# Kernel tuning notes

Measured on AMD Instinct MI355X. Metric: run time of the kernel, lower is better.

## Reference

```python
import jax, jax.numpy as jnp
import numpy as np

N_NODES = 50000
N_EDGES = 1600000
N_GRAPHS = 512
IN_DIM = 128
HID = 128          # nb_hidden
HALF = HID // 2    # per-branch GAT out dim
NEG_SLOPE = 0.2


def _glorot(key, shape):
    fan_in, fan_out = shape[0], shape[-1]
    lim = (6.0 / (fan_in + fan_out)) ** 0.5
    return jax.random.uniform(key, shape, jnp.float32, -lim, lim)


def setup_inputs() -> dict:
    key = jax.random.key(0)
    ks = jax.random.split(key, 32)
    inp = {
        "x": jax.random.normal(ks[0], (N_NODES, IN_DIM), jnp.float32),
        "edge_index": jax.random.randint(ks[1], (2, N_EDGES), 0, N_NODES, jnp.int64),
        "dense_edge_idx": jax.random.randint(ks[2], (2, N_EDGES), 0, N_NODES, jnp.int64),
        "batch": jnp.sort(jax.random.randint(ks[3], (N_NODES,), 0, N_GRAPHS, jnp.int64)),
    }
    # Shared GAT layers (layersB aliases layersA in the source!), nb_layer = 3
    in_dims = [IN_DIM, HID, HID]
    for i, d_in in enumerate(in_dims):
        inp[f"W{i}"] = _glorot(ks[4 + 4 * i], (d_in, HALF))
        inp[f"a_src{i}"] = _glorot(ks[5 + 4 * i], (1, HALF))[0]
        inp[f"a_dst{i}"] = _glorot(ks[6 + 4 * i], (1, HALF))[0]
        inp[f"b{i}"] = jnp.zeros((HALF,), jnp.float32)
    inp["Wf"] = _glorot(ks[20], (HID, 1))
    inp["bf"] = jnp.zeros((1,), jnp.float32)
    return inp


def _gat_conv(x, src, dst, W, a_src, a_dst, b):
    """PyG GATConv, heads=1, concat=True, add_self_loops=True."""
    n = x.shape[0]
    h = x @ W                                   # [N, HALF]
    loops = jnp.arange(n, dtype=src.dtype)
    s = jnp.concatenate([src, loops])           # [E+N]
    d = jnp.concatenate([dst, loops])
    e = (h @ a_src)[s] + (h @ a_dst)[d]         # per-edge raw score
    e = jnp.where(e >= 0, e, NEG_SLOPE * e)     # LeakyReLU(0.2)
    # segment softmax over destination nodes
    m = jax.ops.segment_max(e, d, num_segments=n)
    e = jnp.exp(e - m[d])
    z = jax.ops.segment_sum(e, d, num_segments=n)
    alpha = e / (z[d] + 1e-16)                  # [E+N]
    out = jax.ops.segment_sum(h[s] * alpha[:, None], d, num_segments=n)
    return out + b


def reference(x, edge_index, dense_edge_idx, batch,
              W0, a_src0, a_dst0, b0,
              W1, a_src1, a_dst1, b1,
              W2, a_src2, a_dst2, b2,
              Wf, bf):
    layers = [(W0, a_src0, a_dst0, b0), (W1, a_src1, a_dst1, b1), (W2, a_src2, a_dst2, b2)]
    for (W, a_s, a_d, b) in layers:
        x_A = _gat_conv(x, edge_index[0], edge_index[1], W, a_s, a_d, b)
        x_B = _gat_conv(x, dense_edge_idx[0], dense_edge_idx[1], W, a_s, a_d, b)
        x = jax.nn.relu(jnp.concatenate([x_A, x_B], axis=1))   # [N, HID]
    pooled = jax.ops.segment_sum(x, batch, num_segments=N_GRAPHS)  # [G, HID]
    y = (pooled @ Wf + bf).squeeze(-1)                             # [G]
    return y
```

## Files before the change

### kernel.cpp

```cpp
#include <hip/hip_runtime.h>
#include <hip/hip_bf16.h>
#include <hip/hip_fp16.h>

#define NEG_INF -3.4e38f
#define BCAP 9216

typedef _Float16 f16x8 __attribute__((ext_vector_type(8)));
typedef float f32x4 __attribute__((ext_vector_type(4)));

static __device__ __forceinline__ float leaky(float t) { return t >= 0.f ? t : 0.2f * t; }
static __device__ __forceinline__ __half2 i2h2(int v) { __half2 h; *(int*)&h = v; return h; }

__global__ __launch_bounds__(256) void bucket_k(const int* __restrict__ eiA, const int* __restrict__ eiB,
                                                int E, int nbkt, int* __restrict__ bktCnt,
                                                int* __restrict__ pairs,
                                                const float* __restrict__ W0, const float* __restrict__ W1,
                                                const float* __restrict__ W2, _Float16* __restrict__ Wt) {
    int t = threadIdx.x;
    if (blockIdx.x < 96) {
        int i = blockIdx.x * 256 + t;
        int l = i >> 13;
        int idx = i & 8191;
        int c = idx >> 7;
        int k = idx & 127;
        const float* W = (l == 0) ? W0 : (l == 1) ? W1 : W2;
        Wt[i] = (_Float16)W[k * 64 + c];
    }

    int KB = gridDim.x >> 1;
    int b = blockIdx.x;
    int sel = (b >= KB);
    int bb = sel ? b - KB : b;
    const int* src = sel ? eiB : eiA;
    const int* dst = src + E;
    int* bc = bktCnt + (sel ? nbkt : 0);
    int* pr = pairs + (size_t)(sel ? nbkt : 0) * BCAP;

    __shared__ int hist[256];
    hist[t] = 0;
    __syncthreads();

    int e0 = (int)(((long long)bb * E) / KB);
    int e1 = (int)(((long long)(bb + 1) * E) / KB);
    for (int i = e0 + t; i < e1; i += 256) atomicAdd(&hist[dst[i] >> 8], 1);
    __syncthreads();

    int h = hist[t];
    int base = h ? atomicAdd(&bc[t], h) : 0;
    __syncthreads();
    hist[t] = base;
    __syncthreads();

    for (int i = e0 + t; i < e1; i += 256) {
        int d = dst[i];
        int s = src[i];
        int bk = d >> 8;
        int pos = atomicAdd(&hist[bk], 1);
        if (pos < BCAP) pr[(size_t)bk * BCAP + pos] = s | ((d & 255) << 16);
    }
}

__global__ __launch_bounds__(256) void bscan_k(const int* __restrict__ bktCnt, const int* __restrict__ pairs,
                                               int N, int nbkt, int2* __restrict__ rpl2,
                                               int* __restrict__ bsum) {
    __shared__ int h[256];
    int b = blockIdx.x;
    int sel = (b >= nbkt);
    int bk = sel ? b - nbkt : b;
    const int* bc = bktCnt + (sel ? nbkt : 0);
    const int* pr = pairs + ((size_t)(sel ? nbkt : 0) + bk) * BCAP;
    int t = threadIdx.x;
    h[t] = 0;
    __syncthreads();
    int cb = min(bc[bk], BCAP);
    for (int i = t; i < cb; i += 256) atomicAdd(&h[pr[i] >> 16], 1);
    __syncthreads();
    int v = h[t];
#pragma unroll
    for (int off = 1; off < 256; off <<= 1) {
        int add = (t >= off) ? h[t - off] : 0;
        __syncthreads();
        h[t] += add;
        __syncthreads();
    }
    int node = (bk << 8) + t;
    if (node < N) rpl2[(sel ? N : 0) + node] = make_int2(h[t] - v, v);
    if (t == 255) bsum[b] = h[255];
}

__global__ __launch_bounds__(512) void scan2_k(int* __restrict__ bsum, int nb,
                                               float* __restrict__ y, const float* __restrict__ bf, int G) {
    __shared__ int s[512];
    int t = threadIdx.x;
    for (int g = t; g < G; g += 512) y[g] = bf[0];
    int seg = t >> 8;
    int j = t & 255;
    int v = (j < nb) ? bsum[seg * nb + j] : 0;
    s[t] = v;
    __syncthreads();
#pragma unroll
    for (int off = 1; off < 256; off <<= 1) {
        int add = (j >= off) ? s[t - off] : 0;
        __syncthreads();
        s[t] += add;
        __syncthreads();
    }
    if (j < nb) bsum[seg * nb + j] = s[t] - v;
}

__global__ __launch_bounds__(256) void bfill2_k(const int* __restrict__ bktCnt, const int* __restrict__ pairs,
                                                int N, int nbkt, const int2* __restrict__ rpl2,
                                                const int* __restrict__ bsum, int2* __restrict__ rp2,
                                                int* __restrict__ colA, int* __restrict__ colB) {
    __shared__ int curs[256];
    int b = blockIdx.x;
    int sel = (b >= nbkt);
    int bk = sel ? b - nbkt : b;
    const int* bc = bktCnt + (sel ? nbkt : 0);
    const int* pr = pairs + ((size_t)(sel ? nbkt : 0) + bk) * BCAP;
    int* col = sel ? colB : colA;
    int t = threadIdx.x;
    int base = bsum[b];
    int node = (bk << 8) + t;
    if (node < N) {
        int2 lv = rpl2[(sel ? N : 0) + node];
        int r0 = lv.x + base;
        rp2[(sel ? N : 0) + node] = make_int2(r0, lv.y);
        curs[t] = r0;
    }
    __syncthreads();
    int cb = min(bc[bk], BCAP);
    for (int i = t; i < cb; i += 256) {
        int pk = pr[i];
        int p = atomicAdd(&curs[pk >> 16], 1);
        col[p] = pk & 0xFFFF;
    }
}

template <int IN16>
__global__ __launch_bounds__(256) void gemm_k(const void* __restrict__ Xv, const _Float16* __restrict__ Wt,
                                              const float* __restrict__ asrc, const float* __restrict__ adst,
                                              _Float16* __restrict__ H16, float* __restrict__ es,
                                              float* __restrict__ ed, int N) {
    int tid = threadIdx.x;
    int w = tid >> 6;
    int lane = tid & 63;
    int l15 = lane & 15;
    int hi = lane >> 4;
    int rbase = blockIdx.x * 128 + w * 32;

    f32x4 acc[2][4] = {};
#pragma unroll
    for (int kc = 0; kc < 4; ++kc) {
        f16x8 a[2];
#pragma unroll
        for (int mt = 0; mt < 2; ++mt) {
            int r = min(rbase + mt * 16 + l15, N - 1);
            if (IN16) {
                const _Float16* X = (const _Float16*)Xv;
                a[mt] = *(const f16x8*)(X + (size_t)r * 128 + kc * 32 + hi * 8);
            } else {
                const float* px = (const float*)Xv + (size_t)r * 128 + kc * 32 + hi * 8;
                float4 x0 = *(const float4*)px;
                float4 x1 = *(const float4*)(px + 4);
                f16x8 t;
                t[0] = (_Float16)x0.x; t[1] = (_Float16)x0.y; t[2] = (_Float16)x0.z; t[3] = (_Float16)x0.w;
                t[4] = (_Float16)x1.x; t[5] = (_Float16)x1.y; t[6] = (_Float16)x1.z; t[7] = (_Float16)x1.w;
                a[mt] = t;
            }
        }
#pragma unroll
        for (int nt = 0; nt < 4; ++nt) {
            f16x8 bfrag = *(const f16x8*)(Wt + (size_t)(nt * 16 + l15) * 128 + kc * 32 + hi * 8);
            acc[0][nt] = __builtin_amdgcn_mfma_f32_16x16x32_f16(a[0], bfrag, acc[0][nt], 0, 0, 0);
            acc[1][nt] = __builtin_amdgcn_mfma_f32_16x16x32_f16(a[1], bfrag, acc[1][nt], 0, 0, 0);
        }
    }

    float av[4], dv[4];
#pragma unroll
    for (int nt = 0; nt < 4; ++nt) {
        av[nt] = asrc[nt * 16 + l15];
        dv[nt] = adst[nt * 16 + l15];
    }
#pragma unroll
    for (int mt = 0; mt < 2; ++mt) {
#pragma unroll
        for (int r = 0; r < 4; ++r) {
            int row = rbase + mt * 16 + hi * 4 + r;
            float s1 = 0.f, s2 = 0.f;
#pragma unroll
            for (int nt = 0; nt < 4; ++nt) {
                float v = acc[mt][nt][r];
                s1 += v * av[nt];
                s2 += v * dv[nt];
            }
#pragma unroll
            for (int off = 1; off < 16; off <<= 1) {
                s1 += __shfl_xor(s1, off, 64);
                s2 += __shfl_xor(s2, off, 64);
            }
            if (row < N) {
                if (l15 == 0) { es[row] = s1; ed[row] = s2; }
#pragma unroll
                for (int nt = 0; nt < 4; ++nt)
                    H16[(size_t)row * 64 + nt * 16 + l15] = (_Float16)acc[mt][nt][r];
            }
        }
    }
}

template <int WRITEY>
__global__ __launch_bounds__(256) void agg_k(const __half* __restrict__ h16, const float* __restrict__ es,
                                             const float* __restrict__ ed,
                                             const int2* __restrict__ rp2A, const int* __restrict__ colA,
                                             const int2* __restrict__ rp2B, const int* __restrict__ colB,
                                             const float* __restrict__ bias, __half* __restrict__ xout, int N,
                                             const float* __restrict__ Wf,
                                             float* __restrict__ ydotA, float* __restrict__ ydotB) {
    __shared__ int2 sp[4][64];
    int WBh = gridDim.x >> 1;
    int b = blockIdx.x;
    int sel = (b >= WBh);
    int w = threadIdx.x >> 6;
    int lane = threadIdx.x & 63;
    int wid = (sel ? b - WBh : b) * 4 + w;
    if (wid >= N) return;
    const int2* rp2 = sel ? rp2B : rp2A;
    const int* col = sel ? colB : colA;
    int coff = sel ? 64 : 0;

    int q = lane >> 4;
    int l16 = lane & 15;
    int2 rd = rp2[wid];
    int r0 = rd.x;
    int deg = rd.y;
    int tot = deg + 1;
    float edv = ed[wid];
    const char* hbase = (const char*)h16;
    int loff = l16 * 8;

    __half2 acc01 = __floats2half2_rn(0.f, 0.f);
    __half2 acc23 = __floats2half2_rn(0.f, 0.f);
    float z = 0.f;
    float m;

    if (tot <= 64) {
        int sv = (lane < deg) ? col[r0 + lane] : wid;
        bool valid = (lane < tot);
        float esv = valid ? es[sv] : NEG_INF;
        float mr = esv;
#pragma unroll
        for (int off = 32; off; off >>= 1) mr = fmaxf(mr, __shfl_xor(mr, off, 64));
        m = leaky(mr + edv);
        float p = valid ? __expf(leaky(esv + edv) - m) : 0.f;
        z = p;
        __half2 ph = __floats2half2_rn(p, p);
        sp[w][lane] = make_int2(sv << 7, *(int*)&ph);
        int totr = (tot + 7) & ~7;
        int j = 0;
        for (; j + 16 <= totr; j += 16) {
            int2 e1 = sp[w][j + q];
            int2 e2 = sp[w][j + 4 + q];
            int2 e3 = sp[w][j + 8 + q];
            int2 e4 = sp[w][j + 12 + q];
            uint2 ha = *(const uint2*)(hbase + (unsigned)(e1.x + loff));
            uint2 hb = *(const uint2*)(hbase + (unsigned)(e2.x + loff));
            uint2 hc = *(const uint2*)(hbase + (unsigned)(e3.x + loff));
            uint2 hd = *(const uint2*)(hbase + (unsigned)(e4.x + loff));
            __half2 pa = i2h2(e1.y), pb = i2h2(e2.y), pc = i2h2(e3.y), pd = i2h2(e4.y);
            acc01 = __hfma2(i2h2((int)ha.x), pa, acc01);
            acc23 = __hfma2(i2h2((int)ha.y), pa, acc23);
            acc01 = __hfma2(i2h2((int)hb.x), pb, acc01);
            acc23 = __hfma2(i2h2((int)hb.y), pb, acc23);
            acc01 = __hfma2(i2h2((int)hc.x), pc, acc01);
            acc23 = __hfma2(i2h2((int)hc.y), pc, acc23);
            acc01 = __hfma2(i2h2((int)hd.x), pd, acc01);
            acc23 = __hfma2(i2h2((int)hd.y), pd, acc23);
        }
        for (; j < totr; j += 8) {
            int2 e1 = sp[w][j + q];
            int2 e2 = sp[w][j + 4 + q];
            uint2 ha = *(const uint2*)(hbase + (unsigned)(e1.x + loff));
            uint2 hb = *(const uint2*)(hbase + (unsigned)(e2.x + loff));
            __half2 pa = i2h2(e1.y), pb = i2h2(e2.y);
            acc01 = __hfma2(i2h2((int)ha.x), pa, acc01);
            acc23 = __hfma2(i2h2((int)ha.y), pa, acc23);
            acc01 = __hfma2(i2h2((int)hb.x), pb, acc01);
            acc23 = __hfma2(i2h2((int)hb.y), pb, acc23);
        }
    } else {
        float mr = NEG_INF;
        for (int base = 0; base < tot; base += 64) {
            int vi = base + lane;
            if (vi < tot) {
                int s = (vi < deg) ? col[r0 + vi] : wid;
                mr = fmaxf(mr, es[s]);
            }
        }
#pragma unroll
        for (int off = 32; off; off >>= 1) mr = fmaxf(mr, __shfl_xor(mr, off, 64));
        m = leaky(mr + edv);
        for (int base = 0; base < tot; base += 64) {
            int vi = base + lane;
            bool valid = (vi < tot);
            int sv = valid ? ((vi < deg) ? col[r0 + vi] : wid) : wid;
            float p = valid ? __expf(leaky(es[sv] + edv) - m) : 0.f;
            z += p;
            __half2 ph = __floats2half2_rn(p, p);
            __syncthreads();
            sp[w][lane] = make_int2(sv << 7, *(int*)&ph);
            int cw = min(64, tot - base);
            int cr = (cw + 7) & ~7;
            for (int j = 0; j < cr; j += 8) {
                int2 e1 = sp[w][j + q];
                int2 e2 = sp[w][j + 4 + q];
                uint2 ha = *(const uint2*)(hbase + (unsigned)(e1.x + loff));
                uint2 hb = *(const uint2*)(hbase + (unsigned)(e2.x + loff));
                __half2 pa = i2h2(e1.y), pb = i2h2(e2.y);
                acc01 = __hfma2(i2h2((int)ha.x), pa, acc01);
                acc23 = __hfma2(i2h2((int)ha.y), pa, acc23);
                acc01 = __hfma2(i2h2((int)hb.x), pb, acc01);
                acc23 = __hfma2(i2h2((int)hb.y), pb, acc23);
            }
        }
    }

#pragma unroll
    for (int off = 32; off; off >>= 1) z += __shfl_xor(z, off, 64);
    {
        int t;
        t = __shfl_xor(*(int*)&acc01, 16, 64); acc01 = __hadd2(acc01, i2h2(t));
        t = __shfl_xor(*(int*)&acc23, 16, 64); acc23 = __hadd2(acc23, i2h2(t));
        t = __shfl_xor(*(int*)&acc01, 32, 64); acc01 = __hadd2(acc01, i2h2(t));
        t = __shfl_xor(*(int*)&acc23, 32, 64); acc23 = __hadd2(acc23, i2h2(t));
    }

    if (q == 0) {
        float2 f01 = __half22float2(acc01);
        float2 f23 = __half22float2(acc23);
        float inv = 1.f / (z + 1e-16f);
        float4 b4 = *(const float4*)(bias + l16 * 4);
        float4 o;
        o.x = fmaxf(f01.x * inv + b4.x, 0.f);
        o.y = fmaxf(f01.y * inv + b4.y, 0.f);
        o.z = fmaxf(f23.x * inv + b4.z, 0.f);
        o.w = fmaxf(f23.y * inv + b4.w, 0.f);
        if (!WRITEY) {
            __half2 o01 = __floats2half2_rn(o.x, o.y);
            __half2 o23 = __floats2half2_rn(o.z, o.w);
            uint2 st;
            st.x = *(unsigned*)&o01;
            st.y = *(unsigned*)&o23;
            *(uint2*)(xout + (size_t)wid * 128 + coff + l16 * 4) = st;
        } else {
            float4 w4 = *(const float4*)(Wf + coff + l16 * 4);
            float hd = o.x * w4.x + o.y * w4.y + o.z * w4.z + o.w * w4.w;
            hd += __shfl_xor(hd, 1, 64);
            hd += __shfl_xor(hd, 2, 64);
            hd += __shfl_xor(hd, 4, 64);
            hd += __shfl_xor(hd, 8, 64);
            if (l16 == 0) (sel ? ydotB : ydotA)[wid] = hd;
        }
    }
}

__global__ __launch_bounds__(256) void pool3_k(const float* __restrict__ ydotA, const float* __restrict__ ydotB,
                                               const int* __restrict__ batch, float* __restrict__ y,
                                               int N, int G) {
    __shared__ float gacc[512];
    int t = threadIdx.x;
    if (G <= 512) {
        for (int g = t; g < 512; g += 256) gacc[g] = 0.f;
        __syncthreads();
        int n0 = blockIdx.x * 2048 + t * 8;
        int curg = -1;
        float accv = 0.f;
        for (int i = 0; i < 8; ++i) {
            int n = n0 + i;
            if (n < N) {
                float v = ydotA[n] + ydotB[n];
                int g = batch[n];
                if (g == curg) accv += v;
                else {
                    if (curg >= 0) atomicAdd(&gacc[curg], accv);
                    curg = g;
                    accv = v;
                }
            }
        }
        if (curg >= 0) atomicAdd(&gacc[curg], accv);
        __syncthreads();
        for (int g = t; g < G; g += 256) {
            float v = gacc[g];
            if (v != 0.f) atomicAdd(&y[g], v);
        }
    } else {
        int n0 = blockIdx.x * 2048 + t * 8;
        for (int i = 0; i < 8; ++i) {
            int n = n0 + i;
            if (n < N) atomicAdd(&y[batch[n]], ydotA[n] + ydotB[n]);
        }
    }
}

static inline size_t align256(size_t x) { return (x + 255) & ~(size_t)255; }

extern "C" void kernel_launch(void* const* d_in, const int* in_sizes, int n_in,
                              void* d_out, int out_size, void* d_ws, size_t ws_size,
                              hipStream_t stream) {
    const float* x0    = (const float*)d_in[0];
    const int*   eiA   = (const int*)d_in[1];
    const int*   eiB   = (const int*)d_in[2];
    const int*   batch = (const int*)d_in[3];
    const float* W[3]   = {(const float*)d_in[4],  (const float*)d_in[8],  (const float*)d_in[12]};
    const float* as_[3] = {(const float*)d_in[5],  (const float*)d_in[9],  (const float*)d_in[13]};
    const float* ad_[3] = {(const float*)d_in[6],  (const float*)d_in[10], (const float*)d_in[14]};
    const float* bb[3]  = {(const float*)d_in[7],  (const float*)d_in[11], (const float*)d_in[15]};
    const float* Wf = (const float*)d_in[16];
    const float* bf = (const float*)d_in[17];

    const int N = in_sizes[0] / 128;
    const int E = in_sizes[1] / 2;
    const int G = out_size;
    float* y = (float*)d_out;

    const int nbkt = (N + 255) >> 8;
    const int nb = nbkt;

    char* p = (char*)d_ws;
    int2* rpl2  = (int2*)p; p += align256((size_t)2 * N * 8);
    int2* rp2   = (int2*)p; p += align256((size_t)2 * N * 8);
    int* bsum   = (int*)p;  p += align256((size_t)2 * nb * 4);
    int* bktCnt = (int*)p;  p += align256((size_t)2 * nbkt * 4);
    int* colA   = (int*)p;  p += align256((size_t)E * 4);
    int* colB   = (int*)p;  p += align256((size_t)E * 4);
    _Float16* h16 = (_Float16*)p; p += align256((size_t)N * 64 * 2);
    float* es   = (float*)p; p += align256((size_t)N * 4);
    float* ed   = (float*)p; p += align256((size_t)N * 4);
    float* ydotA = (float*)p; p += align256((size_t)N * 4);
    float* ydotB = (float*)p; p += align256((size_t)N * 4);
    _Float16* Wt = (_Float16*)p; p += align256((size_t)3 * 8192 * 2);
    __half* xb0 = (__half*)p; p += align256((size_t)N * 128 * 2);
    __half* xb1 = (__half*)p; p += align256((size_t)N * 128 * 2);
    int* pairs = (int*)xb0;
    (void)ws_size; (void)n_in;

    const int KB = 256;
    const int WB = (N + 3) / 4;
    const int PB3 = (N + 2047) / 2048;

    hipMemsetAsync(bktCnt, 0, (size_t)2 * nbkt * 4, stream);
    bucket_k<<<2 * KB, 256, 0, stream>>>(eiA, eiB, E, nbkt, bktCnt, pairs, W[0], W[1], W[2], Wt);
    bscan_k<<<2 * nbkt, 256, 0, stream>>>(bktCnt, pairs, N, nbkt, rpl2, bsum);
    scan2_k<<<1, 512, 0, stream>>>(bsum, nb, y, bf, G);
    bfill2_k<<<2 * nbkt, 256, 0, stream>>>(bktCnt, pairs, N, nbkt, rpl2, bsum, rp2, colA, colB);

    const int GB = (N + 127) / 128;
    const int2* rp2A = rp2;
    const int2* rp2B = rp2 + N;
    gemm_k<0><<<GB, 256, 0, stream>>>(x0, Wt, as_[0], ad_[0], h16, es, ed, N);
    agg_k<0><<<2 * WB, 256, 0, stream>>>((const __half*)h16, es, ed, rp2A, colA, rp2B, colB, bb[0], xb0, N,
                                         Wf, ydotA, ydotB);
    gemm_k<1><<<GB, 256, 0, stream>>>(xb0, Wt + 8192, as_[1], ad_[1], h16, es, ed, N);
    agg_k<0><<<2 * WB, 256, 0, stream>>>((const __half*)h16, es, ed, rp2A, colA, rp2B, colB, bb[1], xb1, N,
                                         Wf, ydotA, ydotB);
    gemm_k<1><<<GB, 256, 0, stream>>>(xb1, Wt + 16384, as_[2], ad_[2], h16, es, ed, N);
    agg_k<1><<<2 * WB, 256, 0, stream>>>((const __half*)h16, es, ed, rp2A, colA, rp2B, colB, bb[2],
                                         (__half*)nullptr, N, Wf, ydotA, ydotB);

    pool3_k<<<PB3, 256, 0, stream>>>(ydotA, ydotB, batch, y, N, G);
}
```

Before: 284.8 us.

## Single-pass GAT aggregation with self-score shift, recomputed source scores and packed metadata

```diff
diff --git a/kernel.cpp b/kernel.cpp
--- a/kernel.cpp
+++ b/kernel.cpp
@@ -9,7 +9,11 @@
 typedef float f32x4 __attribute__((ext_vector_type(4)));
 
 static __device__ __forceinline__ float leaky(float t) { return t >= 0.f ? t : 0.2f * t; }
-static __device__ __forceinline__ __half2 i2h2(int v) { __half2 h; *(int*)&h = v; return h; }
+static __device__ __forceinline__ float4 h4tof4(uint2 u) {
+    float2 f01 = __half22float2(*(__half2*)&u.x);
+    float2 f23 = __half22float2(*(__half2*)&u.y);
+    return make_float4(f01.x, f01.y, f23.x, f23.y);
+}
 
 __global__ __launch_bounds__(256) void bucket_k(const int* __restrict__ eiA, const int* __restrict__ eiB,
                                                 int E, int nbkt, int* __restrict__ bktCnt,
@@ -110,7 +114,7 @@
 
 __global__ __launch_bounds__(256) void bfill2_k(const int* __restrict__ bktCnt, const int* __restrict__ pairs,
                                                 int N, int nbkt, const int2* __restrict__ rpl2,
-                                                const int* __restrict__ bsum, int2* __restrict__ rp2,
+                                                const int* __restrict__ bsum, int4* __restrict__ meta,
                                                 int* __restrict__ colA, int* __restrict__ colB) {
     __shared__ int curs[256];
     int b = blockIdx.x;
@@ -125,7 +129,7 @@
     if (node < N) {
         int2 lv = rpl2[(sel ? N : 0) + node];
         int r0 = lv.x + base;
-        rp2[(sel ? N : 0) + node] = make_int2(r0, lv.y);
+        *(int2*)&meta[(sel ? N : 0) + node] = make_int2(r0, lv.y);
         curs[t] = r0;
     }
     __syncthreads();
@@ -140,8 +144,8 @@
 template <int IN16>
 __global__ __launch_bounds__(256) void gemm_k(const void* __restrict__ Xv, const _Float16* __restrict__ Wt,
                                               const float* __restrict__ asrc, const float* __restrict__ adst,
-                                              _Float16* __restrict__ H16, float* __restrict__ es,
-                                              float* __restrict__ ed, int N) {
+                                              _Float16* __restrict__ H16, int4* __restrict__ metaA,
+                                              int4* __restrict__ metaB, int N) {
     int tid = threadIdx.x;
     int w = tid >> 6;
     int lane = tid & 63;
@@ -201,7 +205,11 @@
                 s2 += __shfl_xor(s2, off, 64);
             }
             if (row < N) {
-                if (l15 == 0) { es[row] = s1; ed[row] = s2; }
+                if (l15 == 0) {
+                    float2 sd = make_float2(s1, s2);
+                    *(float2*)((char*)&metaA[row] + 8) = sd;
+                    *(float2*)((char*)&metaB[row] + 8) = sd;
+                }
 #pragma unroll
                 for (int nt = 0; nt < 4; ++nt)
                     H16[(size_t)row * 64 + nt * 16 + l15] = (_Float16)acc[mt][nt][r];
@@ -211,14 +219,13 @@
 }
 
 template <int WRITEY>
-__global__ __launch_bounds__(256) void agg_k(const __half* __restrict__ h16, const float* __restrict__ es,
-                                             const float* __restrict__ ed,
-                                             const int2* __restrict__ rp2A, const int* __restrict__ colA,
-                                             const int2* __restrict__ rp2B, const int* __restrict__ colB,
+__global__ __launch_bounds__(256) void agg_k(const _Float16* __restrict__ h16,
+                                             const float* __restrict__ asrc,
+                                             const int4* __restrict__ metaA, const int* __restrict__ colA,
+                                             const int4* __restrict__ metaB, const int* __restrict__ colB,
                                              const float* __restrict__ bias, __half* __restrict__ xout, int N,
                                              const float* __restrict__ Wf,
                                              float* __restrict__ ydotA, float* __restrict__ ydotB) {
-    __shared__ int2 sp[4][64];
     int WBh = gridDim.x >> 1;
     int b = blockIdx.x;
     int sel = (b >= WBh);
@@ -226,126 +233,85 @@
     int lane = threadIdx.x & 63;
     int wid = (sel ? b - WBh : b) * 4 + w;
     if (wid >= N) return;
-    const int2* rp2 = sel ? rp2B : rp2A;
+    const int4* meta = sel ? metaB : metaA;
     const int* col = sel ? colB : colA;
     int coff = sel ? 64 : 0;
 
     int q = lane >> 4;
     int l16 = lane & 15;
-    int2 rd = rp2[wid];
-    int r0 = rd.x;
-    int deg = rd.y;
-    int tot = deg + 1;
-    float edv = ed[wid];
-    const char* hbase = (const char*)h16;
-    int loff = l16 * 8;
-
-    __half2 acc01 = __floats2half2_rn(0.f, 0.f);
-    __half2 acc23 = __floats2half2_rn(0.f, 0.f);
-    float z = 0.f;
-    float m;
-
-    if (tot <= 64) {
-        int sv = (lane < deg) ? col[r0 + lane] : wid;
-        bool valid = (lane < tot);
-        float esv = valid ? es[sv] : NEG_INF;
-        float mr = esv;
-#pragma unroll
-        for (int off = 32; off; off >>= 1) mr = fmaxf(mr, __shfl_xor(mr, off, 64));
-        m = leaky(mr + edv);
-        float p = valid ? __expf(leaky(esv + edv) - m) : 0.f;
-        z = p;
-        __half2 ph = __floats2half2_rn(p, p);
-        sp[w][lane] = make_int2(sv << 7, *(int*)&ph);
-        int totr = (tot + 7) & ~7;
-        int j = 0;
-        for (; j + 16 <= totr; j += 16) {
-            int2 e1 = sp[w][j + q];
-            int2 e2 = sp[w][j + 4 + q];
-            int2 e3 = sp[w][j + 8 + q];
-            int2 e4 = sp[w][j + 12 + q];
-            uint2 ha = *(const uint2*)(hbase + (unsigned)(e1.x + loff));
-            uint2 hb = *(const uint2*)(hbase + (unsigned)(e2.x + loff));
-            uint2 hc = *(const uint2*)(hbase + (unsigned)(e3.x + loff));
-            uint2 hd = *(const uint2*)(hbase + (unsigned)(e4.x + loff));
-            __half2 pa = i2h2(e1.y), pb = i2h2(e2.y), pc = i2h2(e3.y), pd = i2h2(e4.y);
-            acc01 = __hfma2(i2h2((int)ha.x), pa, acc01);
-            acc23 = __hfma2(i2h2((int)ha.y), pa, acc23);
-            acc01 = __hfma2(i2h2((int)hb.x), pb, acc01);
-            acc23 = __hfma2(i2h2((int)hb.y), pb, acc23);
-            acc01 = __hfma2(i2h2((int)hc.x), pc, acc01);
-            acc23 = __hfma2(i2h2((int)hc.y), pc, acc23);
-            acc01 = __hfma2(i2h2((int)hd.x), pd, acc01);
-            acc23 = __hfma2(i2h2((int)hd.y), pd, acc23);
-        }
-        for (; j < totr; j += 8) {
-            int2 e1 = sp[w][j + q];
-            int2 e2 = sp[w][j + 4 + q];
-            uint2 ha = *(const uint2*)(hbase + (unsigned)(e1.x + loff));
-            uint2 hb = *(const uint2*)(hbase + (unsigned)(e2.x + loff));
-            __half2 pa = i2h2(e1.y), pb = i2h2(e2.y);
-            acc01 = __hfma2(i2h2((int)ha.x), pa, acc01);
-            acc23 = __hfma2(i2h2((int)ha.y), pa, acc23);
-            acc01 = __hfma2(i2h2((int)hb.x), pb, acc01);
-            acc23 = __hfma2(i2h2((int)hb.y), pb, acc23);
-        }
-    } else {
-        float mr = NEG_INF;
-        for (int base = 0; base < tot; base += 64) {
-            int vi = base + lane;
-            if (vi < tot) {
-                int s = (vi < deg) ? col[r0 + vi] : wid;
-                mr = fmaxf(mr, es[s]);
-            }
-        }
-#pragma unroll
-        for (int off = 32; off; off >>= 1) mr = fmaxf(mr, __shfl_xor(mr, off, 64));
-        m = leaky(mr + edv);
-        for (int base = 0; base < tot; base += 64) {
-            int vi = base + lane;
-            bool valid = (vi < tot);
-            int sv = valid ? ((vi < deg) ? col[r0 + vi] : wid) : wid;
-            float p = valid ? __expf(leaky(es[sv] + edv) - m) : 0.f;
-            z += p;
-            __half2 ph = __floats2half2_rn(p, p);
-            __syncthreads();
-            sp[w][lane] = make_int2(sv << 7, *(int*)&ph);
-            int cw = min(64, tot - base);
-            int cr = (cw + 7) & ~7;
-            for (int j = 0; j < cr; j += 8) {
-                int2 e1 = sp[w][j + q];
-                int2 e2 = sp[w][j + 4 + q];
-                uint2 ha = *(const uint2*)(hbase + (unsigned)(e1.x + loff));
-                uint2 hb = *(const uint2*)(hbase + (unsigned)(e2.x + loff));
-                __half2 pa = i2h2(e1.y), pb = i2h2(e2.y);
-                acc01 = __hfma2(i2h2((int)ha.x), pa, acc01);
-                acc23 = __hfma2(i2h2((int)ha.y), pa, acc23);
-                acc01 = __hfma2(i2h2((int)hb.x), pb, acc01);
-                acc23 = __hfma2(i2h2((int)hb.y), pb, acc23);
-            }
-        }
-    }
-
-#pragma unroll
-    for (int off = 32; off; off >>= 1) z += __shfl_xor(z, off, 64);
-    {
-        int t;
-        t = __shfl_xor(*(int*)&acc01, 16, 64); acc01 = __hadd2(acc01, i2h2(t));
-        t = __shfl_xor(*(int*)&acc23, 16, 64); acc23 = __hadd2(acc23, i2h2(t));
-        t = __shfl_xor(*(int*)&acc01, 32, 64); acc01 = __hadd2(acc01, i2h2(t));
-        t = __shfl_xor(*(int*)&acc23, 32, 64); acc23 = __hadd2(acc23, i2h2(t));
-    }
+    int4 mv = meta[wid];
+    int r0 = mv.x;
+    int deg = mv.y;
+    float esv = __int_as_float(mv.z);
+    float edv = __int_as_float(mv.w);
+    float m = leaky(esv + edv);
+    float4 a4 = *(const float4*)(asrc + l16 * 4);
+
+    uint2 hs = *(const uint2*)(h16 + (size_t)wid * 64 + l16 * 4);
+    float4 fs = h4tof4(hs);
+    float ps = (q == 0) ? 1.f : 0.f;
+    float4 acc = make_float4(ps * fs.x, ps * fs.y, ps * fs.z, ps * fs.w);
+    float z = ps;
+
+    if (deg > 0) {
+        int dm1 = deg - 1;
+        int c1 = col[r0 + min(q, dm1)];
+        int c2 = col[r0 + min(4 + q, dm1)];
+        uint2 h1 = *(const uint2*)(h16 + (size_t)c1 * 64 + l16 * 4);
+        uint2 h2 = *(const uint2*)(h16 + (size_t)c2 * 64 + l16 * 4);
+        int n1 = col[r0 + min(8 + q, dm1)];
+        int n2 = col[r0 + min(12 + q, dm1)];
+        for (int j = 0; j < deg; j += 8) {
+            uint2 hn1 = *(const uint2*)(h16 + (size_t)n1 * 64 + l16 * 4);
+            uint2 hn2 = *(const uint2*)(h16 + (size_t)n2 * 64 + l16 * 4);
+            int m1 = col[r0 + min(j + 16 + q, dm1)];
+            int m2 = col[r0 + min(j + 20 + q, dm1)];
+
+            float4 f1 = h4tof4(h1);
+            float4 f2 = h4tof4(h2);
+            float d1 = f1.x * a4.x + f1.y * a4.y + f1.z * a4.z + f1.w * a4.w;
+            float d2 = f2.x * a4.x + f2.y * a4.y + f2.z * a4.z + f2.w * a4.w;
+#pragma unroll
+            for (int off = 1; off < 16; off <<= 1) {
+                d1 += __shfl_xor(d1, off, 64);
+                d2 += __shfl_xor(d2, off, 64);
+            }
+            float p1 = (j + q < deg) ? __expf(leaky(d1 + edv) - m) : 0.f;
+            float p2 = (j + 4 + q < deg) ? __expf(leaky(d2 + edv) - m) : 0.f;
+            z += p1 + p2;
+            acc.x = fmaf(p1, f1.x, acc.x);
+            acc.y = fmaf(p1, f1.y, acc.y);
+            acc.z = fmaf(p1, f1.z, acc.z);
+            acc.w = fmaf(p1, f1.w, acc.w);
+            acc.x = fmaf(p2, f2.x, acc.x);
+            acc.y = fmaf(p2, f2.y, acc.y);
+            acc.z = fmaf(p2, f2.z, acc.z);
+            acc.w = fmaf(p2, f2.w, acc.w);
+
+            h1 = hn1; h2 = hn2;
+            n1 = m1; n2 = m2;
+        }
+    }
+
+    z += __shfl_xor(z, 16, 64);
+    z += __shfl_xor(z, 32, 64);
+    acc.x += __shfl_xor(acc.x, 16, 64);
+    acc.y += __shfl_xor(acc.y, 16, 64);
+    acc.z += __shfl_xor(acc.z, 16, 64);
+    acc.w += __shfl_xor(acc.w, 16, 64);
+    acc.x += __shfl_xor(acc.x, 32, 64);
+    acc.y += __shfl_xor(acc.y, 32, 64);
+    acc.z += __shfl_xor(acc.z, 32, 64);
+    acc.w += __shfl_xor(acc.w, 32, 64);
 
     if (q == 0) {
-        float2 f01 = __half22float2(acc01);
-        float2 f23 = __half22float2(acc23);
         float inv = 1.f / (z + 1e-16f);
         float4 b4 = *(const float4*)(bias + l16 * 4);
         float4 o;
-        o.x = fmaxf(f01.x * inv + b4.x, 0.f);
-        o.y = fmaxf(f01.y * inv + b4.y, 0.f);
-        o.z = fmaxf(f23.x * inv + b4.z, 0.f);
-        o.w = fmaxf(f23.y * inv + b4.w, 0.f);
+        o.x = fmaxf(acc.x * inv + b4.x, 0.f);
+        o.y = fmaxf(acc.y * inv + b4.y, 0.f);
+        o.z = fmaxf(acc.z * inv + b4.z, 0.f);
+        o.w = fmaxf(acc.w * inv + b4.w, 0.f);
         if (!WRITEY) {
             __half2 o01 = __floats2half2_rn(o.x, o.y);
             __half2 o23 = __floats2half2_rn(o.z, o.w);
@@ -430,14 +396,12 @@
 
     char* p = (char*)d_ws;
     int2* rpl2  = (int2*)p; p += align256((size_t)2 * N * 8);
-    int2* rp2   = (int2*)p; p += align256((size_t)2 * N * 8);
+    int4* meta  = (int4*)p; p += align256((size_t)2 * N * 16);
     int* bsum   = (int*)p;  p += align256((size_t)2 * nb * 4);
     int* bktCnt = (int*)p;  p += align256((size_t)2 * nbkt * 4);
     int* colA   = (int*)p;  p += align256((size_t)E * 4);
     int* colB   = (int*)p;  p += align256((size_t)E * 4);
     _Float16* h16 = (_Float16*)p; p += align256((size_t)N * 64 * 2);
-    float* es   = (float*)p; p += align256((size_t)N * 4);
-    float* ed   = (float*)p; p += align256((size_t)N * 4);
     float* ydotA = (float*)p; p += align256((size_t)N * 4);
     float* ydotB = (float*)p; p += align256((size_t)N * 4);
     _Float16* Wt = (_Float16*)p; p += align256((size_t)3 * 8192 * 2);
@@ -454,19 +418,19 @@
     bucket_k<<<2 * KB, 256, 0, stream>>>(eiA, eiB, E, nbkt, bktCnt, pairs, W[0], W[1], W[2], Wt);
     bscan_k<<<2 * nbkt, 256, 0, stream>>>(bktCnt, pairs, N, nbkt, rpl2, bsum);
     scan2_k<<<1, 512, 0, stream>>>(bsum, nb, y, bf, G);
-    bfill2_k<<<2 * nbkt, 256, 0, stream>>>(bktCnt, pairs, N, nbkt, rpl2, bsum, rp2, colA, colB);
+    bfill2_k<<<2 * nbkt, 256, 0, stream>>>(bktCnt, pairs, N, nbkt, rpl2, bsum, meta, colA, colB);
 
     const int GB = (N + 127) / 128;
-    const int2* rp2A = rp2;
-    const int2* rp2B = rp2 + N;
-    gemm_k<0><<<GB, 256, 0, stream>>>(x0, Wt, as_[0], ad_[0], h16, es, ed, N);
-    agg_k<0><<<2 * WB, 256, 0, stream>>>((const __half*)h16, es, ed, rp2A, colA, rp2B, colB, bb[0], xb0, N,
+    int4* metaA = meta;
+    int4* metaB = meta + N;
+    gemm_k<0><<<GB, 256, 0, stream>>>(x0, Wt, as_[0], ad_[0], h16, metaA, metaB, N);
+    agg_k<0><<<2 * WB, 256, 0, stream>>>(h16, as_[0], metaA, colA, metaB, colB, bb[0], xb0, N,
                                          Wf, ydotA, ydotB);
-    gemm_k<1><<<GB, 256, 0, stream>>>(xb0, Wt + 8192, as_[1], ad_[1], h16, es, ed, N);
-    agg_k<0><<<2 * WB, 256, 0, stream>>>((const __half*)h16, es, ed, rp2A, colA, rp2B, colB, bb[1], xb1, N,
+    gemm_k<1><<<GB, 256, 0, stream>>>(xb0, Wt + 8192, as_[1], ad_[1], h16, metaA, metaB, N);
+    agg_k<0><<<2 * WB, 256, 0, stream>>>(h16, as_[1], metaA, colA, metaB, colB, bb[1], xb1, N,
                                          Wf, ydotA, ydotB);
-    gemm_k<1><<<GB, 256, 0, stream>>>(xb1, Wt + 16384, as_[2], ad_[2], h16, es, ed, N);
-    agg_k<1><<<2 * WB, 256, 0, stream>>>((const __half*)h16, es, ed, rp2A, colA, rp2B, colB, bb[2],
+    gemm_k<1><<<GB, 256, 0, stream>>>(xb1, Wt + 16384, as_[2], ad_[2], h16, metaA, metaB, N);
+    agg_k<1><<<2 * WB, 256, 0, stream>>>(h16, as_[2], metaA, colA, metaB, colB, bb[2],
                                          (__half*)nullptr, N, Wf, ydotA, ydotB);
 
     pool3_k<<<PB3, 256, 0, stream>>>(ydotA, ydotB, batch, y, N, G);
```

After: 335.3 us. +17.7%, slower.
